# Kernel tuning notes

Hardware: AMD Instinct MI355X
Metric: run time of the kernel (lower is better)

## Reference

```python
import jax, jax.numpy as jnp
import numpy as np

NBINS = 256

def _rescale_0_1(img):
    return (img + 1.0) * (127.0 / 255.0)

def _rescale_back(img):
    return img * (255.0 / 127.0) - 1.0

def _rgb_to_yuv_y(img):
    # tf.image.rgb_to_yuv luma coefficients; only Y channel is used downstream
    return img[..., 0] * 0.299 + img[..., 1] * 0.587 + img[..., 2] * 0.114

def _equalize_histogram(image):
    # tf.histogram_fixed_width over [0,1] with 256 bins (values clipped to range)
    idx = jnp.clip((image * NBINS).astype(jnp.int32), 0, NBINS - 1)
    hist = jnp.zeros((NBINS,), jnp.int32).at[idx.reshape(-1)].add(1)
    cdf = jnp.cumsum(hist)
    cdf_min = jnp.min(cdf)
    pix_cnt = image.shape[0] * image.shape[1]
    return (cdf - cdf_min).astype(jnp.float32) / jnp.float32(pix_cnt - 1)

def _interpolate(dx, dy, x):
    # brute-force searchsorted substitute: first index where dx - x > 0
    del_vals = dx[jnp.newaxis, :] - x[:, jnp.newaxis]          # [N, 256]
    ind_1 = jnp.argmax(jnp.sign(del_vals), axis=1)             # first positive
    ind_0 = jnp.clip(ind_1 - 1, 0, NBINS - 1)
    dx0, dx1 = dx[ind_0], dx[ind_1]
    dy0, dy1 = dy[ind_0], dy[ind_1]
    denom = dx1 - dx0
    safe_denom = jnp.where(denom == 0, jnp.float32(1.0), denom)
    interp = dy0 + (dy1 - dy0) * (x - dx0) / safe_denom
    return jnp.where(x <= dx[0], dy[0], jnp.where(x >= dx[-1], dy[-1], interp))

def setup_inputs() -> dict:
    key = jax.random.key(0)
    k1, k2 = jax.random.split(key)
    H, W = 1024, 1024
    src = jax.random.uniform(k1, (H, W, 3), jnp.float32, minval=-1.0, maxval=1.0)
    tgt = jax.random.uniform(k2, (H, W, 3), jnp.float32, minval=-1.0, maxval=1.0)
    return {"src": src, "tgt": tgt}

def reference(src, tgt):
    src = _rescale_0_1(src)
    tgt = _rescale_0_1(tgt)
    tgt_y = _rgb_to_yuv_y(tgt)
    h, w = src.shape[0], src.shape[1]
    floating_space = jnp.clip(jnp.arange(0.0, 1.00001, 1.0 / 255.0, dtype=jnp.float32), 0.0, 1.0)
    source = src[:, :, 0]
    cdfsrc = _equalize_histogram(source)
    cdftgt = _equalize_histogram(tgt_y)
    pxmap = _interpolate(cdftgt, floating_space, cdfsrc)
    pxmap = _interpolate(floating_space, pxmap, source.reshape(h * w))
    pxmap = pxmap.reshape(h, w, 1)
    res = jnp.clip(pxmap, 0.0, 1.0)
    return _rescale_back(res)
```

## Files before the change

kernel.cpp:

```cpp
#include <hip/hip_runtime.h>

#define NBINS 256

__device__ __forceinline__ float fs_val(int j) {
    const float c = (float)(1.0 / 255.0);
    float v = (float)j * c;
    return v > 1.0f ? 1.0f : v;
}

__device__ __forceinline__ int bin_of(float s) {
    int i = (int)(s * 256.0f);
    i = i < 0 ? 0 : i;
    i = i > NBINS - 1 ? NBINS - 1 : i;
    return i;
}

__global__ void hm_hist(const float* __restrict__ src,
                        const float* __restrict__ tgt,
                        int* __restrict__ histS, int* __restrict__ histT,
                        int nquad) {
    __shared__ int hs[NBINS];
    __shared__ int ht[NBINS];
    for (int i = threadIdx.x; i < NBINS; i += blockDim.x) { hs[i] = 0; ht[i] = 0; }
    __syncthreads();

    const float c1 = (float)(127.0 / 255.0);
    int tid = blockIdx.x * blockDim.x + threadIdx.x;
    int stride = gridDim.x * blockDim.x;

    for (int q = tid; q < nquad; q += stride) {
        const float4* s4 = (const float4*)(src + 12 * (size_t)q);
        float4 a = s4[0], b = s4[1], c = s4[2];
        float p0 = (a.x + 1.0f) * c1;
        float p1 = (a.w + 1.0f) * c1;
        float p2 = (b.z + 1.0f) * c1;
        float p3 = (c.y + 1.0f) * c1;
        atomicAdd(&hs[bin_of(p0)], 1);
        atomicAdd(&hs[bin_of(p1)], 1);
        atomicAdd(&hs[bin_of(p2)], 1);
        atomicAdd(&hs[bin_of(p3)], 1);

        const float4* t4 = (const float4*)(tgt + 12 * (size_t)q);
        float4 ta = t4[0], tb = t4[1], tc = t4[2];
        {
            float r = (ta.x + 1.0f) * c1, g = (ta.y + 1.0f) * c1, bb = (ta.z + 1.0f) * c1;
            float y = r * 0.299f + g * 0.587f + bb * 0.114f;
            atomicAdd(&ht[bin_of(y)], 1);
        }
        {
            float r = (ta.w + 1.0f) * c1, g = (tb.x + 1.0f) * c1, bb = (tb.y + 1.0f) * c1;
            float y = r * 0.299f + g * 0.587f + bb * 0.114f;
            atomicAdd(&ht[bin_of(y)], 1);
        }
        {
            float r = (tb.z + 1.0f) * c1, g = (tb.w + 1.0f) * c1, bb = (tc.x + 1.0f) * c1;
            float y = r * 0.299f + g * 0.587f + bb * 0.114f;
            atomicAdd(&ht[bin_of(y)], 1);
        }
        {
            float r = (tc.y + 1.0f) * c1, g = (tc.z + 1.0f) * c1, bb = (tc.w + 1.0f) * c1;
            float y = r * 0.299f + g * 0.587f + bb * 0.114f;
            atomicAdd(&ht[bin_of(y)], 1);
        }
    }
    __syncthreads();
    for (int i = threadIdx.x; i < NBINS; i += blockDim.x) {
        if (hs[i]) atomicAdd(&histS[i], hs[i]);
        if (ht[i]) atomicAdd(&histT[i], ht[i]);
    }
}

__global__ void hm_cdf_map(const int* __restrict__ histS,
                           const int* __restrict__ histT,
                           float* __restrict__ pxmap, int npix) {
    __shared__ int sS[NBINS];
    __shared__ int sT[NBINS];
    __shared__ float cdfT[NBINS];
    int t = threadIdx.x;
    sS[t] = histS[t];
    sT[t] = histT[t];
    __syncthreads();
    for (int off = 1; off < NBINS; off <<= 1) {
        int vS = sS[t], vT = sT[t];
        int aS = (t >= off) ? sS[t - off] : 0;
        int aT = (t >= off) ? sT[t - off] : 0;
        __syncthreads();
        sS[t] = vS + aS;
        sT[t] = vT + aT;
        __syncthreads();
    }
    int minS = sS[0], minT = sT[0];
    float denomN = (float)(npix - 1);
    float xS = (float)(sS[t] - minS) / denomN;
    cdfT[t] = (float)(sT[t] - minT) / denomN;
    __syncthreads();

    float res;
    if (xS <= cdfT[0]) {
        res = fs_val(0);
    } else if (xS >= cdfT[NBINS - 1]) {
        res = fs_val(NBINS - 1);
    } else {
        int lo = 0, hi = NBINS - 1;
        while (hi - lo > 1) {
            int mid = (lo + hi) >> 1;
            if (cdfT[mid] > xS) hi = mid; else lo = mid;
        }
        int j1 = hi, j0 = hi - 1;
        float dx0 = cdfT[j0], dx1 = cdfT[j1];
        float dy0 = fs_val(j0), dy1 = fs_val(j1);
        res = dy0 + (dy1 - dy0) * (xS - dx0) / (dx1 - dx0);
    }
    pxmap[t] = res;
}

__global__ void hm_apply(const float* __restrict__ src,
                         const float* __restrict__ pxmap,
                         float* __restrict__ out, int nquad) {
    __shared__ float pm[NBINS];
    for (int i = threadIdx.x; i < NBINS; i += blockDim.x) pm[i] = pxmap[i];
    __syncthreads();

    const float c1 = (float)(127.0 / 255.0);
    const float c2 = (float)(255.0 / 127.0);
    int tid = blockIdx.x * blockDim.x + threadIdx.x;
    int stride = gridDim.x * blockDim.x;

    for (int q = tid; q < nquad; q += stride) {
        const float4* s4 = (const float4*)(src + 12 * (size_t)q);
        float4 a = s4[0], b = s4[1], c = s4[2];
        float xs0 = a.x, xs1 = a.w, xs2 = b.z, xs3 = c.y;
        float4 o;
        float xv[4] = {xs0, xs1, xs2, xs3};
        float ov[4];
        #pragma unroll
        for (int k = 0; k < 4; ++k) {
            float x = (xv[k] + 1.0f) * c1;
            float r;
            if (x <= 0.0f) {
                r = pm[0];
            } else if (x >= 1.0f) {
                r = pm[NBINS - 1];
            } else {
                int g = (int)(x * 255.0f) + 1;
                g = g < 1 ? 1 : (g > NBINS - 1 ? NBINS - 1 : g);
                while (g < NBINS - 1 && fs_val(g) <= x) ++g;
                while (g > 1 && fs_val(g - 1) > x) --g;
                int j1 = g, j0 = g - 1;
                float dx0 = fs_val(j0), dx1 = fs_val(j1);
                r = pm[j0] + (pm[j1] - pm[j0]) * (x - dx0) / (dx1 - dx0);
            }
            r = r < 0.0f ? 0.0f : (r > 1.0f ? 1.0f : r);
            ov[k] = r * c2 - 1.0f;
        }
        o.x = ov[0]; o.y = ov[1]; o.z = ov[2]; o.w = ov[3];
        ((float4*)out)[q] = o;
    }
}

extern "C" void kernel_launch(void* const* d_in, const int* in_sizes, int n_in,
                              void* d_out, int out_size, void* d_ws, size_t ws_size,
                              hipStream_t stream) {
    const float* src = (const float*)d_in[0];
    const float* tgt = (const float*)d_in[1];
    float* out = (float*)d_out;

    int npix = out_size;
    int nquad = npix >> 2;

    int* histS = (int*)d_ws;
    int* histT = histS + NBINS;
    float* pxmap = (float*)(histT + NBINS);

    hipMemsetAsync(d_ws, 0, 2 * NBINS * sizeof(int), stream);

    hm_hist<<<256, 256, 0, stream>>>(src, tgt, histS, histT, nquad);

    hm_cdf_map<<<1, NBINS, 0, stream>>>(histS, histT, pxmap, npix);

    int blocks = (nquad + 255) / 256;
    hm_apply<<<blocks, 256, 0, stream>>>(src, pxmap, out, nquad);
}
```

Measured before the change: 83.98 us.

## Replace global histogram atomics with per-block partials reduced in CDF kernel

The histogram kernel now writes each block's shared-memory histogram to a separate partial slot instead of atomically adding into a global histogram, and the grid grows from 256 to 512 blocks. The CDF kernel runs 1024 threads that sum the 512 partials per bin before the scan, which removes the memset launch and the global atomics. In exchange the single-block CDF kernel reads 2×512×256 ints serially, which may lengthen that stage. There is also a __syncthreads inside divergent branches, which relies on both branches reaching a barrier.

```diff
diff --git a/kernel.cpp b/kernel.cpp
--- a/kernel.cpp
+++ b/kernel.cpp
@@ -1,6 +1,7 @@
 #include <hip/hip_runtime.h>
 
 #define NBINS 256
+#define HBLK 512
 
 __device__ __forceinline__ float fs_val(int j) {
     const float c = (float)(1.0 / 255.0);
@@ -17,7 +18,7 @@
 
 __global__ void hm_hist(const float* __restrict__ src,
                         const float* __restrict__ tgt,
-                        int* __restrict__ histS, int* __restrict__ histT,
+                        int* __restrict__ partS, int* __restrict__ partT,
                         int nquad) {
     __shared__ int hs[NBINS];
     __shared__ int ht[NBINS];
@@ -44,74 +45,89 @@
         float4 ta = t4[0], tb = t4[1], tc = t4[2];
         {
             float r = (ta.x + 1.0f) * c1, g = (ta.y + 1.0f) * c1, bb = (ta.z + 1.0f) * c1;
-            float y = r * 0.299f + g * 0.587f + bb * 0.114f;
-            atomicAdd(&ht[bin_of(y)], 1);
+            atomicAdd(&ht[bin_of(r * 0.299f + g * 0.587f + bb * 0.114f)], 1);
         }
         {
             float r = (ta.w + 1.0f) * c1, g = (tb.x + 1.0f) * c1, bb = (tb.y + 1.0f) * c1;
-            float y = r * 0.299f + g * 0.587f + bb * 0.114f;
-            atomicAdd(&ht[bin_of(y)], 1);
+            atomicAdd(&ht[bin_of(r * 0.299f + g * 0.587f + bb * 0.114f)], 1);
         }
         {
             float r = (tb.z + 1.0f) * c1, g = (tb.w + 1.0f) * c1, bb = (tc.x + 1.0f) * c1;
-            float y = r * 0.299f + g * 0.587f + bb * 0.114f;
-            atomicAdd(&ht[bin_of(y)], 1);
+            atomicAdd(&ht[bin_of(r * 0.299f + g * 0.587f + bb * 0.114f)], 1);
         }
         {
             float r = (tc.y + 1.0f) * c1, g = (tc.z + 1.0f) * c1, bb = (tc.w + 1.0f) * c1;
-            float y = r * 0.299f + g * 0.587f + bb * 0.114f;
-            atomicAdd(&ht[bin_of(y)], 1);
+            atomicAdd(&ht[bin_of(r * 0.299f + g * 0.587f + bb * 0.114f)], 1);
         }
     }
     __syncthreads();
     for (int i = threadIdx.x; i < NBINS; i += blockDim.x) {
-        if (hs[i]) atomicAdd(&histS[i], hs[i]);
-        if (ht[i]) atomicAdd(&histT[i], ht[i]);
+        partS[(size_t)blockIdx.x * NBINS + i] = hs[i];
+        partT[(size_t)blockIdx.x * NBINS + i] = ht[i];
     }
 }
 
-__global__ void hm_cdf_map(const int* __restrict__ histS,
-                           const int* __restrict__ histT,
-                           float* __restrict__ pxmap, int npix) {
+__global__ void __launch_bounds__(1024)
+hm_cdf_map(const int* __restrict__ partS,
+           const int* __restrict__ partT,
+           float* __restrict__ pxmap, int npix) {
     __shared__ int sS[NBINS];
     __shared__ int sT[NBINS];
     __shared__ float cdfT[NBINS];
     int t = threadIdx.x;
-    sS[t] = histS[t];
-    sT[t] = histT[t];
+    int bin = t & (NBINS - 1);
+    int split = t >> 8;
+
+    if (t < NBINS) { sS[t] = 0; sT[t] = 0; }
     __syncthreads();
+
+    int accS = 0, accT = 0;
+    for (int b = split; b < HBLK; b += 4) {
+        accS += partS[(size_t)b * NBINS + bin];
+        accT += partT[(size_t)b * NBINS + bin];
+    }
+    atomicAdd(&sS[bin], accS);
+    atomicAdd(&sT[bin], accT);
+    __syncthreads();
+
     for (int off = 1; off < NBINS; off <<= 1) {
-        int vS = sS[t], vT = sT[t];
-        int aS = (t >= off) ? sS[t - off] : 0;
-        int aT = (t >= off) ? sT[t - off] : 0;
+        int vS = 0, vT = 0, aS = 0, aT = 0;
+        if (t < NBINS) {
+            vS = sS[t]; vT = sT[t];
+            if (t >= off) { aS = sS[t - off]; aT = sT[t - off]; }
+        }
         __syncthreads();
-        sS[t] = vS + aS;
-        sT[t] = vT + aT;
+        if (t < NBINS) { sS[t] = vS + aS; sT[t] = vT + aT; }
         __syncthreads();
     }
-    int minS = sS[0], minT = sT[0];
-    float denomN = (float)(npix - 1);
-    float xS = (float)(sS[t] - minS) / denomN;
-    cdfT[t] = (float)(sT[t] - minT) / denomN;
-    __syncthreads();
 
-    float res;
-    if (xS <= cdfT[0]) {
-        res = fs_val(0);
-    } else if (xS >= cdfT[NBINS - 1]) {
-        res = fs_val(NBINS - 1);
+    if (t < NBINS) {
+        int minS = sS[0], minT = sT[0];
+        float denomN = (float)(npix - 1);
+        float xS = (float)(sS[t] - minS) / denomN;
+        cdfT[t] = (float)(sT[t] - minT) / denomN;
+        __syncthreads();
+
+        float res;
+        if (xS <= cdfT[0]) {
+            res = fs_val(0);
+        } else if (xS >= cdfT[NBINS - 1]) {
+            res = fs_val(NBINS - 1);
+        } else {
+            int lo = 0, hi = NBINS - 1;
+            while (hi - lo > 1) {
+                int mid = (lo + hi) >> 1;
+                if (cdfT[mid] > xS) hi = mid; else lo = mid;
+            }
+            int j1 = hi, j0 = hi - 1;
+            float dx0 = cdfT[j0], dx1 = cdfT[j1];
+            float dy0 = fs_val(j0), dy1 = fs_val(j1);
+            res = dy0 + (dy1 - dy0) * (xS - dx0) / (dx1 - dx0);
+        }
+        pxmap[t] = res;
     } else {
-        int lo = 0, hi = NBINS - 1;
-        while (hi - lo > 1) {
-            int mid = (lo + hi) >> 1;
-            if (cdfT[mid] > xS) hi = mid; else lo = mid;
-        }
-        int j1 = hi, j0 = hi - 1;
-        float dx0 = cdfT[j0], dx1 = cdfT[j1];
-        float dy0 = fs_val(j0), dy1 = fs_val(j1);
-        res = dy0 + (dy1 - dy0) * (xS - dx0) / (dx1 - dx0);
+        __syncthreads();
     }
-    pxmap[t] = res;
 }
 
 __global__ void hm_apply(const float* __restrict__ src,
@@ -129,9 +145,7 @@
     for (int q = tid; q < nquad; q += stride) {
         const float4* s4 = (const float4*)(src + 12 * (size_t)q);
         float4 a = s4[0], b = s4[1], c = s4[2];
-        float xs0 = a.x, xs1 = a.w, xs2 = b.z, xs3 = c.y;
-        float4 o;
-        float xv[4] = {xs0, xs1, xs2, xs3};
+        float xv[4] = {a.x, a.w, b.z, c.y};
         float ov[4];
         #pragma unroll
         for (int k = 0; k < 4; ++k) {
@@ -153,6 +167,7 @@
             r = r < 0.0f ? 0.0f : (r > 1.0f ? 1.0f : r);
             ov[k] = r * c2 - 1.0f;
         }
+        float4 o;
         o.x = ov[0]; o.y = ov[1]; o.z = ov[2]; o.w = ov[3];
         ((float4*)out)[q] = o;
     }
@@ -168,16 +183,11 @@
     int npix = out_size;
     int nquad = npix >> 2;
 
-    int* histS = (int*)d_ws;
-    int* histT = histS + NBINS;
-    float* pxmap = (float*)(histT + NBINS);
+    int* partS = (int*)d_ws;
+    int* partT = partS + (size_t)HBLK * NBINS;
+    float* pxmap = (float*)(partT + (size_t)HBLK * NBINS);
 
-    hipMemsetAsync(d_ws, 0, 2 * NBINS * sizeof(int), stream);
-
-    hm_hist<<<256, 256, 0, stream>>>(src, tgt, histS, histT, nquad);
-
-    hm_cdf_map<<<1, NBINS, 0, stream>>>(histS, histT, pxmap, npix);
-
-    int blocks = (nquad + 255) / 256;
-    hm_apply<<<blocks, 256, 0, stream>>>(src, pxmap, out, nquad);
+    hm_hist<<<HBLK, 256, 0, stream>>>(src, tgt, partS, partT, nquad);
+    hm_cdf_map<<<1, 1024, 0, stream>>>(partS, partT, pxmap, npix);
+    hm_apply<<<(nquad + 255) / 256, 256, 0, stream>>>(src, pxmap, out, nquad);
 }
```

New measurement: 89.12 us. +6.1%, slower.
